# Kernel tuning notes

Measured on AMD Instinct MI355X. Metric: run time of the kernel, lower is better.

The kernel has to match this reference:

```python
import jax, jax.numpy as jnp
import numpy as np
import math

D_MODEL = 1024
H = 16
D_K = D_MODEL // H
B = 4
S = 2048
NEG = -1e9


def setup_inputs() -> dict:
    key = jax.random.key(0)
    ks = jax.random.split(key, 11)
    scale = 1.0 / math.sqrt(D_MODEL)
    inp = {
        'q': jax.random.normal(ks[0], (B, S, D_MODEL), dtype=jnp.float32),
        'k': jax.random.normal(ks[1], (B, S, D_MODEL), dtype=jnp.float32),
        'v': jax.random.normal(ks[2], (B, S, D_MODEL), dtype=jnp.float32),
        'wq': jax.random.normal(ks[3], (D_MODEL, D_MODEL), dtype=jnp.float32) * scale,
        'bq': jnp.zeros((D_MODEL,), dtype=jnp.float32),
        'wk': jax.random.normal(ks[4], (D_MODEL, D_MODEL), dtype=jnp.float32) * scale,
        'bk': jnp.zeros((D_MODEL,), dtype=jnp.float32),
        'wv': jax.random.normal(ks[5], (D_MODEL, D_MODEL), dtype=jnp.float32) * scale,
        'bv': jnp.zeros((D_MODEL,), dtype=jnp.float32),
        'wo': jax.random.normal(ks[6], (D_MODEL, D_MODEL), dtype=jnp.float32) * scale,
        'bo': jnp.zeros((D_MODEL,), dtype=jnp.float32),
        # broadcastable causal mask [1, 1, S, S]; 0 = masked out
        'mask': jnp.tril(jnp.ones((S, S), dtype=jnp.int32))[None, None, :, :],
    }
    return inp


def reference(q, k, v, wq, bq, wk, bk, wv, bv, wo, bo, mask):
    # QKV projections: x @ W^T + b (nn.Linear convention)
    def split_heads(x):  # [B, S, D] -> [B, H, S, d_k]
        return x.reshape(B, S, H, D_K).transpose(0, 2, 1, 3)

    query = split_heads(q @ wq.T + bq)
    key_ = split_heads(k @ wk.T + bk)
    value = split_heads(v @ wv.T + bv)

    # scaled dot-product attention with mask; scores: [B, H, S, S]
    scores = jnp.einsum('bhqd,bhkd->bhqk', query, key_) / math.sqrt(D_K)
    scores = jnp.where(mask == 0, jnp.float32(NEG), scores)
    attn = jax.nn.softmax(scores, axis=-1)
    ctx = jnp.einsum('bhqk,bhkd->bhqd', attn, value)  # [B, H, S, d_k]

    # merge heads and output projection
    ctx = ctx.transpose(0, 2, 1, 3).reshape(B, S, D_MODEL)
    return ctx @ wo.T + bo
```

## Files before the change

kernel.cpp:

```cpp
#include <hip/hip_runtime.h>

#define DEVI __device__ __forceinline__

typedef __attribute__((ext_vector_type(8))) __bf16 bf16x8;
typedef __attribute__((ext_vector_type(4))) float f32x4;
typedef __attribute__((ext_vector_type(16))) float f32x16;
typedef __attribute__((ext_vector_type(4))) unsigned uint32x4;

DEVI __bf16 f2bf(float f) {
  unsigned u = __builtin_bit_cast(unsigned, f);
  unsigned r = u + 0x7fffu + ((u >> 16) & 1u);
  unsigned short h = (unsigned short)(r >> 16);
  return __builtin_bit_cast(__bf16, h);
}

DEVI unsigned cvt_pk_bf16(float lo, float hi) {
  unsigned r;
  asm("v_cvt_pk_bf16_f32 %0, %1, %2" : "=v"(r) : "v"(lo), "v"(hi));
  return r;
}

DEVI void load_lds16(const void* g, void* l) {
  __builtin_amdgcn_global_load_lds((__attribute__((address_space(1))) const void*)g,
                                   (__attribute__((address_space(3))) void*)l,
                                   16, 0, 0);
}

__global__ void convert_bf16(const float* __restrict__ in, __bf16* __restrict__ out, int n8) {
  int stride = gridDim.x * blockDim.x;
  for (int i = blockIdx.x * blockDim.x + threadIdx.x; i < n8; i += stride) {
    float4 a = ((const float4*)in)[i * 2];
    float4 b = ((const float4*)in)[i * 2 + 1];
    bf16x8 o;
    o[0] = f2bf(a.x); o[1] = f2bf(a.y); o[2] = f2bf(a.z); o[3] = f2bf(a.w);
    o[4] = f2bf(b.x); o[5] = f2bf(b.y); o[6] = f2bf(b.z); o[7] = f2bf(b.w);
    ((bf16x8*)out)[i] = o;
  }
}

__global__ void convert_w4(const float* __restrict__ w0, const float* __restrict__ w1,
                           const float* __restrict__ w2, const float* __restrict__ w3,
                           __bf16* __restrict__ o0, __bf16* __restrict__ o1,
                           __bf16* __restrict__ o2, __bf16* __restrict__ o3, int n8) {
  int stride = gridDim.x * blockDim.x;
  for (int i = blockIdx.x * blockDim.x + threadIdx.x; i < 4 * n8; i += stride) {
    int sel = i / n8, j = i - sel * n8;
    const float* in = sel == 0 ? w0 : sel == 1 ? w1 : sel == 2 ? w2 : w3;
    __bf16* out = sel == 0 ? o0 : sel == 1 ? o1 : sel == 2 ? o2 : o3;
    float4 a = ((const float4*)in)[j * 2];
    float4 b = ((const float4*)in)[j * 2 + 1];
    bf16x8 o;
    o[0] = f2bf(a.x); o[1] = f2bf(a.y); o[2] = f2bf(a.z); o[3] = f2bf(a.w);
    o[4] = f2bf(b.x); o[5] = f2bf(b.y); o[6] = f2bf(b.z); o[7] = f2bf(b.w);
    ((bf16x8*)out)[j] = o;
  }
}

template<int MODE>
__global__ __launch_bounds__(256, 2) void gemm_bt(
    const __bf16* __restrict__ A, const __bf16* __restrict__ W,
    const float* __restrict__ bias, void* __restrict__ outp)
{
  __shared__ __bf16 As[3][128 * 32];
  __shared__ __bf16 Bs[3][128 * 32];
  const int tid = threadIdx.x;
  const int lane = tid & 63;
  const int ln = lane & 15, g = lane >> 4;
  const int w = tid >> 6;
  const int wr = w >> 1, wc = w & 1;
  const int id = blockIdx.y * 64 + blockIdx.x;
  const int bx = 8 * (id & 7) + ((id >> 3) & 7);
  const int by = id >> 6;
  const int row0 = bx * 128, col0 = by * 128;

  f32x4 acc[4][4] = {};

  auto stage = [&](int buf, int kt) {
    const int k0 = kt * 32;
#pragma unroll
    for (int i = 0; i < 2; ++i) {
      int c = tid + 256 * i;
      int r = c >> 2, sl = c & 3;
      int so = 8 * (sl ^ ((r >> 1) & 3));
      load_lds16(&A[(size_t)(row0 + r) * 1024 + k0 + so], &As[buf][c * 8]);
      load_lds16(&W[(size_t)(col0 + r) * 1024 + k0 + so], &Bs[buf][c * 8]);
    }
  };

  auto compute = [&](int buf) {
    const __bf16* as = As[buf];
    const __bf16* bs = Bs[buf];
    bf16x8 aF[4], bF[4];
#pragma unroll
    for (int mi = 0; mi < 4; ++mi) {
      int r = wr * 64 + mi * 16 + ln;
      aF[mi] = *(const bf16x8*)&as[r * 32 + ((g * 8) ^ (((r >> 1) & 3) * 8))];
    }
#pragma unroll
    for (int ni = 0; ni < 4; ++ni) {
      int r = wc * 64 + ni * 16 + ln;
      bF[ni] = *(const bf16x8*)&bs[r * 32 + ((g * 8) ^ (((r >> 1) & 3) * 8))];
    }
    __builtin_amdgcn_s_setprio(1);
#pragma unroll
    for (int mi = 0; mi < 4; ++mi)
#pragma unroll
      for (int ni = 0; ni < 4; ++ni)
        acc[mi][ni] = __builtin_amdgcn_mfma_f32_16x16x32_bf16(aF[mi], bF[ni], acc[mi][ni], 0, 0, 0);
    __builtin_amdgcn_s_setprio(0);
  };

  stage(0, 0);
  stage(1, 1);
#pragma unroll 1
  for (int kt = 0; kt < 31; ++kt) {
    asm volatile("s_waitcnt vmcnt(4)" ::: "memory");
    __builtin_amdgcn_s_barrier();
    asm volatile("" ::: "memory");
    if (kt + 2 < 32) stage((kt + 2) % 3, kt + 2);
    compute(kt % 3);
  }
  asm volatile("s_waitcnt vmcnt(0)" ::: "memory");
  __builtin_amdgcn_s_barrier();
  asm volatile("" ::: "memory");
  compute(31 % 3);

#pragma unroll
  for (int ni = 0; ni < 4; ++ni) {
    int n = col0 + wc * 64 + ni * 16 + ln;
    float bv = bias[n];
#pragma unroll
    for (int mi = 0; mi < 4; ++mi) {
#pragma unroll
      for (int i = 0; i < 4; ++i) {
        int m = row0 + wr * 64 + mi * 16 + g * 4 + i;
        float val = acc[mi][ni][i] + bv;
        if (MODE == 2) {
          ((float*)outp)[(size_t)m * 1024 + n] = val;
        } else {
          int b = m >> 11, s = m & 2047, h = n >> 6, d = n & 63;
          size_t idx = (MODE == 0)
            ? ((size_t)((b * 16 + h) * 2048 + s) * 64 + d)
            : ((size_t)((b * 16 + h) * 64 + d) * 2048 + s);
          ((__bf16*)outp)[idx] = f2bf(val);
        }
      }
    }
  }
}

__global__ __launch_bounds__(512, 4) void attn_fwd(
    const __bf16* __restrict__ Qh, const __bf16* __restrict__ Kh,
    const __bf16* __restrict__ Vt, __bf16* __restrict__ Ctx)
{
  __shared__ __bf16 KVs[8][64 * 64];

  const int tid = threadIdx.x;
  const int lane = tid & 63;
  const int l31 = lane & 31, hl = lane >> 5;
  const int w = tid >> 6;
  const int wq3 = w & 3, p = w >> 2;
  const int bh = blockIdx.x;
  const int b = bh >> 4, h = bh & 15;
  const float CE = 0.18033688f;
  const float MC = 40.0f * CE;

  auto stagePair = [&](int tp) {
    const int base = 2 * (tp & 1);
    const int c = tid;
    const int r = c >> 3, sl = c & 7;
    const int so = 8 * (sl ^ (r & 7));
#pragma unroll
    for (int i = 0; i < 2; ++i) {
      const int kv0 = (2 * tp + i) * 64, s = base + i;
      load_lds16(&Kh[((size_t)bh * 2048 + kv0 + r) * 64 + so], &KVs[s][c * 8]);
      load_lds16(&Vt[((size_t)bh * 64 + r) * 2048 + kv0 + so], &KVs[4 + s][c * 8]);
    }
  };

  auto strip = [&](int qb) {
    const int q0 = qb * 128;
    const int qw = q0 + wq3 * 32;
    const int qglob = qw + l31;
    const int np = qb + 1;

    bf16x8 qF[4];
#pragma unroll
    for (int ds = 0; ds < 4; ++ds)
      qF[ds] = *(const bf16x8*)&Qh[((size_t)bh * 2048 + qglob) * 64 + ds * 16 + hl * 8];

    f32x16 oT[2] = {};
    float lrun = 0.f;

    __syncthreads();
    stagePair(0);
    for (int tp = 0; tp < np; ++tp) {
      __syncthreads();
      if (tp + 1 < np) stagePair(tp + 1);
      const int kv0 = (2 * tp + p) * 64;
      if (kv0 > qw + 31) continue;
      const __bf16* ksm = KVs[2 * (tp & 1) + p];
      const __bf16* vsm = KVs[4 + 2 * (tp & 1) + p];

      f32x16 sT[2] = {};
#pragma unroll
      for (int kblk = 0; kblk < 2; ++kblk) {
        bf16x8 aK[4];
        const int r = kblk * 32 + l31;
#pragma unroll
        for (int ds = 0; ds < 4; ++ds)
          aK[ds] = *(const bf16x8*)&ksm[r * 64 + ((ds * 16 + hl * 8) ^ ((r & 7) * 8))];
        __builtin_amdgcn_s_setprio(1);
#pragma unroll
        for (int ds = 0; ds < 4; ++ds)
          sT[kblk] = __builtin_amdgcn_mfma_f32_32x32x16_bf16(aK[ds], qF[ds], sT[kblk], 0, 0, 0);
        __builtin_amdgcn_s_setprio(0);
      }

      if (kv0 + 63 > qw) {
#pragma unroll
        for (int kblk = 0; kblk < 2; ++kblk)
#pragma unroll
          for (int r = 0; r < 16; ++r) {
            int kvg = kv0 + kblk * 32 + (r & 3) + 8 * (r >> 2) + 4 * hl;
            sT[kblk][r] = (kvg <= qglob) ? sT[kblk][r] : -3e38f;
          }
      }

      unsigned c0[8], c1[8];
      float ps0 = 0.f, ps1 = 0.f, ps2 = 0.f, ps3 = 0.f;
#pragma unroll
      for (int w2 = 0; w2 < 8; ++w2) {
        float p0 = exp2f(__builtin_fmaf(sT[0][2 * w2],     CE, -MC));
        float p1 = exp2f(__builtin_fmaf(sT[0][2 * w2 + 1], CE, -MC));
        float p2 = exp2f(__builtin_fmaf(sT[1][2 * w2],     CE, -MC));
        float p3 = exp2f(__builtin_fmaf(sT[1][2 * w2 + 1], CE, -MC));
        ps0 += p0; ps1 += p1; ps2 += p2; ps3 += p3;
        c0[w2] = cvt_pk_bf16(p0, p1);
        c1[w2] = cvt_pk_bf16(p2, p3);
      }
      lrun += (ps0 + ps1) + (ps2 + ps3);

      uint32x4 Wv[4];
#pragma unroll
      for (int kblk = 0; kblk < 2; ++kblk)
#pragma unroll
        for (int ksl = 0; ksl < 2; ++ksl)
#pragma unroll
          for (int al = 0; al < 2; ++al) {
            unsigned cp = kblk ? c1[4 * ksl + al]     : c0[4 * ksl + al];
            unsigned cq = kblk ? c1[4 * ksl + 2 + al] : c0[4 * ksl + 2 + al];
            unsigned cqx = __shfl_xor(cq, 32);
            unsigned cpx = __shfl_xor(cp, 32);
            Wv[kblk * 2 + ksl][al]     = hl ? cqx : cp;
            Wv[kblk * 2 + ksl][al + 2] = hl ? cq  : cpx;
          }

#pragma unroll
      for (int dblk = 0; dblk < 2; ++dblk) {
        bf16x8 aV[4];
        const int r = dblk * 32 + l31;
#pragma unroll
        for (int ks = 0; ks < 4; ++ks)
          aV[ks] = *(const bf16x8*)&vsm[r * 64 + ((ks * 16 + hl * 8) ^ ((r & 7) * 8))];
        __builtin_amdgcn_s_setprio(1);
#pragma unroll
        for (int ks = 0; ks < 4; ++ks)
          oT[dblk] = __builtin_amdgcn_mfma_f32_32x32x16_bf16(
              aV[ks], __builtin_bit_cast(bf16x8, Wv[ks]), oT[dblk], 0, 0, 0);
        __builtin_amdgcn_s_setprio(0);
      }
    }

    __syncthreads();
    float* ex = (float*)KVs + wq3 * 2176 + lane * 34;
    if (p == 1) {
      lrun += __shfl_xor(lrun, 32);
#pragma unroll
      for (int dblk = 0; dblk < 2; ++dblk)
#pragma unroll
        for (int rb = 0; rb < 8; ++rb)
          *(float2*)(ex + dblk * 16 + rb * 2) =
              make_float2(oT[dblk][2 * rb], oT[dblk][2 * rb + 1]);
      ex[32] = lrun;
    }
    __syncthreads();
    if (p == 0) {
      lrun += __shfl_xor(lrun, 32);
      lrun += ex[32];
#pragma unroll
      for (int dblk = 0; dblk < 2; ++dblk)
#pragma unroll
        for (int rb = 0; rb < 8; ++rb) {
          float2 v = *(float2*)(ex + dblk * 16 + rb * 2);
          oT[dblk][2 * rb]     += v.x;
          oT[dblk][2 * rb + 1] += v.y;
        }
      const float inv = 1.0f / fmaxf(lrun, 1e-30f);
#pragma unroll
      for (int dblk = 0; dblk < 2; ++dblk)
#pragma unroll
        for (int rb = 0; rb < 4; ++rb) {
          unsigned u0 = cvt_pk_bf16(oT[dblk][4 * rb]     * inv, oT[dblk][4 * rb + 1] * inv);
          unsigned u1 = cvt_pk_bf16(oT[dblk][4 * rb + 2] * inv, oT[dblk][4 * rb + 3] * inv);
          int d = dblk * 32 + rb * 8 + 4 * hl;
          size_t idx = ((size_t)(b * 2048 + qglob)) * 1024 + h * 64 + d;
          *(uint2*)&Ctx[idx] = make_uint2(u0, u1);
        }
    }
  };

  strip(15 - (int)blockIdx.y);
  strip((int)blockIdx.y);
}

extern "C" void kernel_launch(void* const* d_in, const int* in_sizes, int n_in,
                              void* d_out, int out_size, void* d_ws, size_t ws_size,
                              hipStream_t stream) {
  const float* q  = (const float*)d_in[0];
  const float* k  = (const float*)d_in[1];
  const float* v  = (const float*)d_in[2];
  const float* wq = (const float*)d_in[3];
  const float* bq = (const float*)d_in[4];
  const float* wk = (const float*)d_in[5];
  const float* bk = (const float*)d_in[6];
  const float* wv = (const float*)d_in[7];
  const float* bv = (const float*)d_in[8];
  const float* wo = (const float*)d_in[9];
  const float* bo = (const float*)d_in[10];
  float* out = (float*)d_out;
  char* ws = (char*)d_ws;

  const size_t MB = 1024 * 1024;
  __bf16* Wqb  = (__bf16*)(ws + 0 * MB);
  __bf16* Wkb  = (__bf16*)(ws + 2 * MB);
  __bf16* Wvb  = (__bf16*)(ws + 4 * MB);
  __bf16* Wob  = (__bf16*)(ws + 6 * MB);
  __bf16* Abuf = (__bf16*)(ws + 8 * MB);
  __bf16* Qh   = (__bf16*)(ws + 24 * MB);
  __bf16* Kh   = (__bf16*)(ws + 40 * MB);
  __bf16* Vt   = (__bf16*)(ws + 56 * MB);
  __bf16* Ctx  = Abuf;

  const int W8 = 1024 * 1024 / 8;
  const int X8 = 8192 * 1024 / 8;
  auto cgrid = [](int n8) { int nb = (n8 + 255) / 256; return dim3((unsigned)(nb < 2048 ? nb : 2048)); };

  convert_w4<<<2048, 256, 0, stream>>>(wq, wk, wv, wo, Wqb, Wkb, Wvb, Wob, W8);

  dim3 ggrid(64, 8);
  convert_bf16<<<cgrid(X8), 256, 0, stream>>>(q, Abuf, X8);
  gemm_bt<0><<<ggrid, 256, 0, stream>>>(Abuf, Wqb, bq, Qh);
  convert_bf16<<<cgrid(X8), 256, 0, stream>>>(k, Abuf, X8);
  gemm_bt<0><<<ggrid, 256, 0, stream>>>(Abuf, Wkb, bk, Kh);
  convert_bf16<<<cgrid(X8), 256, 0, stream>>>(v, Abuf, X8);
  gemm_bt<1><<<ggrid, 256, 0, stream>>>(Abuf, Wvb, bv, Vt);

  attn_fwd<<<dim3(64, 8), 512, 0, stream>>>(Qh, Kh, Vt, Ctx);
  gemm_bt<2><<<ggrid, 256, 0, stream>>>(Ctx, Wob, bo, out);
}
```

Measured before the change: 205.0 us.

## Fuse fp32-to-bf16 input conversion into a single batched QKV projection GEMM

Removes the three standalone activation conversion kernels and three separate projection GEMMs. A new kernel loads fp32 activations into registers, converts them to bf16 while writing LDS, and handles Q, K and V through a z-dimension grid in one launch. This saves the round trip of the bf16 activation buffer through memory and some launch overhead. In exchange, A-tile loads go through registers instead of direct-to-LDS, with double rather than triple buffering, and the epilogue stores scalar bf16 values.

```diff
diff --git a/kernel.cpp b/kernel.cpp
--- a/kernel.cpp
+++ b/kernel.cpp
@@ -24,18 +24,6 @@
   __builtin_amdgcn_global_load_lds((__attribute__((address_space(1))) const void*)g,
                                    (__attribute__((address_space(3))) void*)l,
                                    16, 0, 0);
-}
-
-__global__ void convert_bf16(const float* __restrict__ in, __bf16* __restrict__ out, int n8) {
-  int stride = gridDim.x * blockDim.x;
-  for (int i = blockIdx.x * blockDim.x + threadIdx.x; i < n8; i += stride) {
-    float4 a = ((const float4*)in)[i * 2];
-    float4 b = ((const float4*)in)[i * 2 + 1];
-    bf16x8 o;
-    o[0] = f2bf(a.x); o[1] = f2bf(a.y); o[2] = f2bf(a.z); o[3] = f2bf(a.w);
-    o[4] = f2bf(b.x); o[5] = f2bf(b.y); o[6] = f2bf(b.z); o[7] = f2bf(b.w);
-    ((bf16x8*)out)[i] = o;
-  }
 }
 
 __global__ void convert_w4(const float* __restrict__ w0, const float* __restrict__ w1,
@@ -56,6 +44,118 @@
   }
 }
 
+__global__ __launch_bounds__(256, 3) void gemm_qkv(
+    const float* __restrict__ qa, const float* __restrict__ ka, const float* __restrict__ va,
+    const __bf16* __restrict__ Wq, const __bf16* __restrict__ Wk, const __bf16* __restrict__ Wv,
+    const float* __restrict__ bq, const float* __restrict__ bk, const float* __restrict__ bv,
+    __bf16* __restrict__ Qh, __bf16* __restrict__ Kh, __bf16* __restrict__ Vt)
+{
+  __shared__ __align__(16) __bf16 As[2][128 * 32];
+  __shared__ __align__(16) __bf16 Bs[2][128 * 32];
+  const int sel = blockIdx.z;
+  const float* A = sel == 0 ? qa : sel == 1 ? ka : va;
+  const __bf16* W = sel == 0 ? Wq : sel == 1 ? Wk : Wv;
+  const float* bias = sel == 0 ? bq : sel == 1 ? bk : bv;
+  __bf16* outp = sel == 0 ? Qh : sel == 1 ? Kh : Vt;
+  const bool vmode = (sel == 2);
+
+  const int tid = threadIdx.x;
+  const int lane = tid & 63;
+  const int ln = lane & 15, g = lane >> 4;
+  const int w = tid >> 6;
+  const int wr = w >> 1, wc = w & 1;
+  const int id = blockIdx.y * 64 + blockIdx.x;
+  const int bx = 8 * (id & 7) + ((id >> 3) & 7);
+  const int by = id >> 6;
+  const int row0 = bx * 128, col0 = by * 128;
+
+  const int ar = tid >> 1, ah = tid & 1;
+  const int axr = (ar >> 1) & 3;
+
+  f32x4 acc[4][4] = {};
+  float4 fA[4];
+
+  auto issueA = [&](int kt) {
+    const float4* src = (const float4*)&A[(size_t)(row0 + ar) * 1024 + kt * 32 + ah * 16];
+#pragma unroll
+    for (int j = 0; j < 4; ++j) fA[j] = src[j];
+  };
+  auto issueW = [&](int buf, int kt) {
+#pragma unroll
+    for (int i = 0; i < 2; ++i) {
+      int c = tid + 256 * i;
+      int r = c >> 2, sl = c & 3;
+      int so = 8 * (sl ^ ((r >> 1) & 3));
+      load_lds16(&W[(size_t)(col0 + r) * 1024 + kt * 32 + so], &Bs[buf][c * 8]);
+    }
+  };
+  auto writeA = [&](int buf) {
+#pragma unroll
+    for (int j = 0; j < 2; ++j) {
+      uint32x4 o;
+      o[0] = cvt_pk_bf16(fA[2 * j].x, fA[2 * j].y);
+      o[1] = cvt_pk_bf16(fA[2 * j].z, fA[2 * j].w);
+      o[2] = cvt_pk_bf16(fA[2 * j + 1].x, fA[2 * j + 1].y);
+      o[3] = cvt_pk_bf16(fA[2 * j + 1].z, fA[2 * j + 1].w);
+      int s = 2 * ah + j;
+      *(uint32x4*)&As[buf][ar * 32 + (s ^ axr) * 8] = o;
+    }
+  };
+  auto compute = [&](int buf) {
+    const __bf16* as = As[buf];
+    const __bf16* bs = Bs[buf];
+    bf16x8 aF[4], bF[4];
+#pragma unroll
+    for (int mi = 0; mi < 4; ++mi) {
+      int r = wr * 64 + mi * 16 + ln;
+      aF[mi] = *(const bf16x8*)&as[r * 32 + ((g * 8) ^ (((r >> 1) & 3) * 8))];
+    }
+#pragma unroll
+    for (int ni = 0; ni < 4; ++ni) {
+      int r = wc * 64 + ni * 16 + ln;
+      bF[ni] = *(const bf16x8*)&bs[r * 32 + ((g * 8) ^ (((r >> 1) & 3) * 8))];
+    }
+    __builtin_amdgcn_s_setprio(1);
+#pragma unroll
+    for (int mi = 0; mi < 4; ++mi)
+#pragma unroll
+      for (int ni = 0; ni < 4; ++ni)
+        acc[mi][ni] = __builtin_amdgcn_mfma_f32_16x16x32_bf16(aF[mi], bF[ni], acc[mi][ni], 0, 0, 0);
+    __builtin_amdgcn_s_setprio(0);
+  };
+
+  issueA(0); issueW(0, 0);
+  writeA(0);
+  __syncthreads();
+#pragma unroll 1
+  for (int kt = 0; kt < 32; ++kt) {
+    const int cur = kt & 1, nxt = cur ^ 1;
+    if (kt + 1 < 32) { issueA(kt + 1); issueW(nxt, kt + 1); }
+    compute(cur);
+    if (kt + 1 < 32) writeA(nxt);
+    __syncthreads();
+  }
+
+#pragma unroll
+  for (int ni = 0; ni < 4; ++ni) {
+    int n = col0 + wc * 64 + ni * 16 + ln;
+    float bv = bias[n];
+#pragma unroll
+    for (int mi = 0; mi < 4; ++mi) {
+#pragma unroll
+      for (int i = 0; i < 4; ++i) {
+        int m = row0 + wr * 64 + mi * 16 + g * 4 + i;
+        float val = acc[mi][ni][i] + bv;
+        int b = m >> 11, s = m & 2047, h = n >> 6, d = n & 63;
+        size_t idx = vmode
+          ? ((size_t)((b * 16 + h) * 64 + d) * 2048 + s)
+          : ((size_t)((b * 16 + h) * 2048 + s) * 64 + d);
+        outp[idx] = f2bf(val);
+      }
+    }
+  }
+}
+
 template<int MODE>
 __global__ __launch_bounds__(256, 2) void gemm_bt(
     const __bf16* __restrict__ A, const __bf16* __restrict__ W,
@@ -336,26 +436,19 @@
   __bf16* Wkb  = (__bf16*)(ws + 2 * MB);
   __bf16* Wvb  = (__bf16*)(ws + 4 * MB);
   __bf16* Wob  = (__bf16*)(ws + 6 * MB);
-  __bf16* Abuf = (__bf16*)(ws + 8 * MB);
+  __bf16* Ctx  = (__bf16*)(ws + 8 * MB);
   __bf16* Qh   = (__bf16*)(ws + 24 * MB);
   __bf16* Kh   = (__bf16*)(ws + 40 * MB);
   __bf16* Vt   = (__bf16*)(ws + 56 * MB);
-  __bf16* Ctx  = Abuf;
 
   const int W8 = 1024 * 1024 / 8;
-  const int X8 = 8192 * 1024 / 8;
-  auto cgrid = [](int n8) { int nb = (n8 + 255) / 256; return dim3((unsigned)(nb < 2048 ? nb : 2048)); };
 
   convert_w4<<<2048, 256, 0, stream>>>(wq, wk, wv, wo, Wqb, Wkb, Wvb, Wob, W8);
 
-  dim3 ggrid(64, 8);
-  convert_bf16<<<cgrid(X8), 256, 0, stream>>>(q, Abuf, X8);
-  gemm_bt<0><<<ggrid, 256, 0, stream>>>(Abuf, Wqb, bq, Qh);
-  convert_bf16<<<cgrid(X8), 256, 0, stream>>>(k, Abuf, X8);
-  gemm_bt<0><<<ggrid, 256, 0, stream>>>(Abuf, Wkb, bk, Kh);
-  convert_bf16<<<cgrid(X8), 256, 0, stream>>>(v, Abuf, X8);
-  gemm_bt<1><<<ggrid, 256, 0, stream>>>(Abuf, Wvb, bv, Vt);
+  gemm_qkv<<<dim3(64, 8, 3), 256, 0, stream>>>(q, k, v, Wqb, Wkb, Wvb,
+                                               bq, bk, bv, Qh, Kh, Vt);
 
   attn_fwd<<<dim3(64, 8), 512, 0, stream>>>(Qh, Kh, Vt, Ctx);
-  gemm_bt<2><<<ggrid, 256, 0, stream>>>(Ctx, Wob, bo, out);
-}
+
+  gemm_bt<2><<<dim3(64, 8), 256, 0, stream>>>(Ctx, Wob, bo, out);
+}
```

New measurement: 204.5 us. Within noise of the previous version (-0.2%).

## Enlarge projection GEMM tile to 256x128 with 512 threads and unroll k-loop

Applied to the files above, without the earlier changes.

The projection GEMM now computes a 256x128 output tile per block using 8 waves, up from 128x128 with 4 waves. The grid halves to 256 blocks, one per CU, and each weight tile loaded into LDS is reused across twice as many rows. The k-loop is unrolled by three so triple-buffer indices are compile-time constants, and the wait count is lowered to 3 to match three loads per stage. The swizzled block-index mapping is dropped and LDS use per block grows, which can hurt L2 locality and leaves no spare blocks to balance load.

```diff
diff --git a/kernel.cpp b/kernel.cpp
--- a/kernel.cpp
+++ b/kernel.cpp
@@ -56,22 +56,19 @@
   }
 }
 
-template<int MODE>
-__global__ __launch_bounds__(256, 2) void gemm_bt(
+template<int SEL>
+__global__ __launch_bounds__(512, 2) void gemm_big(
     const __bf16* __restrict__ A, const __bf16* __restrict__ W,
     const float* __restrict__ bias, void* __restrict__ outp)
 {
-  __shared__ __bf16 As[3][128 * 32];
+  __shared__ __bf16 As[3][256 * 32];
   __shared__ __bf16 Bs[3][128 * 32];
   const int tid = threadIdx.x;
   const int lane = tid & 63;
   const int ln = lane & 15, g = lane >> 4;
   const int w = tid >> 6;
   const int wr = w >> 1, wc = w & 1;
-  const int id = blockIdx.y * 64 + blockIdx.x;
-  const int bx = 8 * (id & 7) + ((id >> 3) & 7);
-  const int by = id >> 6;
-  const int row0 = bx * 128, col0 = by * 128;
+  const int row0 = blockIdx.x * 256, col0 = blockIdx.y * 128;
 
   f32x4 acc[4][4] = {};
 
@@ -79,10 +76,15 @@
     const int k0 = kt * 32;
 #pragma unroll
     for (int i = 0; i < 2; ++i) {
-      int c = tid + 256 * i;
+      int c = tid + 512 * i;
       int r = c >> 2, sl = c & 3;
       int so = 8 * (sl ^ ((r >> 1) & 3));
       load_lds16(&A[(size_t)(row0 + r) * 1024 + k0 + so], &As[buf][c * 8]);
+    }
+    {
+      int c = tid;
+      int r = c >> 2, sl = c & 3;
+      int so = 8 * (sl ^ ((r >> 1) & 3));
       load_lds16(&W[(size_t)(col0 + r) * 1024 + k0 + so], &Bs[buf][c * 8]);
     }
   };
@@ -110,20 +112,31 @@
     __builtin_amdgcn_s_setprio(0);
   };
 
+#define GB_STEP(KT, B) \
+  asm volatile("s_waitcnt vmcnt(3)" ::: "memory"); \
+  __builtin_amdgcn_s_barrier(); \
+  asm volatile("" ::: "memory"); \
+  stage(((B) + 2) % 3, (KT) + 2); \
+  compute(B);
+
   stage(0, 0);
   stage(1, 1);
 #pragma unroll 1
-  for (int kt = 0; kt < 31; ++kt) {
-    asm volatile("s_waitcnt vmcnt(4)" ::: "memory");
-    __builtin_amdgcn_s_barrier();
-    asm volatile("" ::: "memory");
-    if (kt + 2 < 32) stage((kt + 2) % 3, kt + 2);
-    compute(kt % 3);
+  for (int u = 0; u < 10; ++u) {
+    const int kt = 3 * u;
+    GB_STEP(kt + 0, 0)
+    GB_STEP(kt + 1, 1)
+    GB_STEP(kt + 2, 2)
   }
+  asm volatile("s_waitcnt vmcnt(3)" ::: "memory");
+  __builtin_amdgcn_s_barrier();
+  asm volatile("" ::: "memory");
+  compute(0);
   asm volatile("s_waitcnt vmcnt(0)" ::: "memory");
   __builtin_amdgcn_s_barrier();
   asm volatile("" ::: "memory");
-  compute(31 % 3);
+  compute(1);
+#undef GB_STEP
 
 #pragma unroll
   for (int ni = 0; ni < 4; ++ni) {
@@ -135,13 +148,13 @@
       for (int i = 0; i < 4; ++i) {
         int m = row0 + wr * 64 + mi * 16 + g * 4 + i;
         float val = acc[mi][ni][i] + bv;
-        if (MODE == 2) {
+        if (SEL == 3) {
           ((float*)outp)[(size_t)m * 1024 + n] = val;
         } else {
           int b = m >> 11, s = m & 2047, h = n >> 6, d = n & 63;
-          size_t idx = (MODE == 0)
-            ? ((size_t)((b * 16 + h) * 2048 + s) * 64 + d)
-            : ((size_t)((b * 16 + h) * 64 + d) * 2048 + s);
+          size_t idx = (SEL == 2)
+            ? ((size_t)((b * 16 + h) * 64 + d) * 2048 + s)
+            : ((size_t)((b * 16 + h) * 2048 + s) * 64 + d);
           ((__bf16*)outp)[idx] = f2bf(val);
         }
       }
@@ -348,14 +361,15 @@
 
   convert_w4<<<2048, 256, 0, stream>>>(wq, wk, wv, wo, Wqb, Wkb, Wvb, Wob, W8);
 
-  dim3 ggrid(64, 8);
+  dim3 ggrid(32, 8);
   convert_bf16<<<cgrid(X8), 256, 0, stream>>>(q, Abuf, X8);
-  gemm_bt<0><<<ggrid, 256, 0, stream>>>(Abuf, Wqb, bq, Qh);
+  gemm_big<0><<<ggrid, 512, 0, stream>>>(Abuf, Wqb, bq, Qh);
   convert_bf16<<<cgrid(X8), 256, 0, stream>>>(k, Abuf, X8);
-  gemm_bt<0><<<ggrid, 256, 0, stream>>>(Abuf, Wkb, bk, Kh);
+  gemm_big<1><<<ggrid, 512, 0, stream>>>(Abuf, Wkb, bk, Kh);
   convert_bf16<<<cgrid(X8), 256, 0, stream>>>(v, Abuf, X8);
-  gemm_bt<1><<<ggrid, 256, 0, stream>>>(Abuf, Wvb, bv, Vt);
+  gemm_big<2><<<ggrid, 512, 0, stream>>>(Abuf, Wvb, bv, Vt);
 
   attn_fwd<<<dim3(64, 8), 512, 0, stream>>>(Qh, Kh, Vt, Ctx);
-  gemm_bt<2><<<ggrid, 256, 0, stream>>>(Ctx, Wob, bo, out);
-}
+
+  gemm_big<3><<<ggrid, 512, 0, stream>>>(Ctx, Wob, bo, out);
+}
```

After: 217.8 us. 6.3% more time.
